# Optimization experiments

Measured on AMD Instinct MI355X. Metric: run time of the kernel, lower is better.

## Reference

```python
import jax, jax.numpy as jnp
import numpy as np

N = 100000      # nodes
E = 1600000     # edges
G = 64          # graphs in batch
H = 128         # hidden (== num_features)
L = 4           # num_layers
C = 16          # num_classes
NCAND = 100000  # candidate edges
BN_EPS = 1e-5


def setup_inputs() -> dict:
    key = jax.random.key(0)
    ks = jax.random.split(key, 24)
    s = 0.05
    inp = {}
    inp["x"] = jax.random.normal(ks[0], (N, H), dtype=jnp.float32)
    inp["edge_index"] = jax.random.randint(ks[1], (2, E), 0, N)
    inp["batch"] = jnp.sort(jax.random.randint(ks[2], (N,), 0, G))
    inp["candidate_edges"] = jax.random.randint(ks[3], (2, NCAND), 0, N)
    # GIN conv params, stacked over L layers (all layers are H->H since num_features==hidden)
    inp["cW1"] = jax.random.normal(ks[4], (L, H, H), dtype=jnp.float32) * s
    inp["cb1"] = jnp.zeros((L, H), jnp.float32)
    inp["cW2"] = jax.random.normal(ks[5], (L, H, H), dtype=jnp.float32) * s
    inp["cb2"] = jnp.zeros((L, H), jnp.float32)
    inp["cgamma"] = jnp.ones((L, H), jnp.float32)
    inp["cbeta"] = jnp.zeros((L, H), jnp.float32)
    inp["ceps"] = jnp.zeros((L,), jnp.float32)  # train_eps=True, init 0
    # node classifier: L*H -> 2H -> H -> H -> C (dropout is identity in eval)
    inp["ncW1"] = jax.random.normal(ks[6], (L * H, 2 * H), dtype=jnp.float32) * s
    inp["ncb1"] = jnp.zeros((2 * H,), jnp.float32)
    inp["ncW2"] = jax.random.normal(ks[7], (2 * H, H), dtype=jnp.float32) * s
    inp["ncb2"] = jnp.zeros((H,), jnp.float32)
    inp["ncW3"] = jax.random.normal(ks[8], (H, H), dtype=jnp.float32) * s
    inp["ncb3"] = jnp.zeros((H,), jnp.float32)
    inp["ncW4"] = jax.random.normal(ks[9], (H, C), dtype=jnp.float32) * s
    inp["ncb4"] = jnp.zeros((C,), jnp.float32)
    # edge predictor: 2*L*H -> 2H -> H -> 1
    inp["epW1"] = jax.random.normal(ks[10], (2 * L * H, 2 * H), dtype=jnp.float32) * s
    inp["epb1"] = jnp.zeros((2 * H,), jnp.float32)
    inp["epW2"] = jax.random.normal(ks[11], (2 * H, H), dtype=jnp.float32) * s
    inp["epb2"] = jnp.zeros((H,), jnp.float32)
    inp["epW3"] = jax.random.normal(ks[12], (H, 1), dtype=jnp.float32) * s
    inp["epb3"] = jnp.zeros((1,), jnp.float32)
    return inp


def _forward(x, cW1, cb1, cW2, cb2, cgamma, cbeta, ceps,
             ncW1, ncb1, ncW2, ncb2, ncW3, ncb3, ncW4, ncb4,
             epW1, epb1, epW2, epb2, epW3, epb3,
             edge_index, batch, candidate_edges):
    src, dst = edge_index[0], edge_index[1]
    h = x
    xs = []
    for l in range(L):
        # GIN: (1+eps)*x_i + sum_{j->i} x_j  (scatter-add over destination nodes)
        agg = jax.ops.segment_sum(h[src], dst, num_segments=N)
        z = (1.0 + ceps[l]) * h + agg
        z = jax.nn.relu(z @ cW1[l] + cb1[l])
        z = jax.nn.relu(z @ cW2[l] + cb2[l])
        # BatchNorm1d (training-mode batch statistics, biased variance)
        mu = z.mean(axis=0)
        var = jnp.var(z, axis=0)
        h = (z - mu) * jax.lax.rsqrt(var + BN_EPS) * cgamma[l] + cbeta[l]
        xs.append(h)
    emb = jnp.concatenate(xs, axis=-1)  # [N, L*H]
    # global mean pool over graphs
    sums = jax.ops.segment_sum(emb, batch, num_segments=G)
    cnt = jax.ops.segment_sum(jnp.ones((N, 1), emb.dtype), batch, num_segments=G)
    gemb = sums / jnp.maximum(cnt, 1.0)  # [G, L*H]
    t = jax.nn.relu(gemb @ ncW1 + ncb1)
    t = jax.nn.relu(t @ ncW2 + ncb2)
    t = jax.nn.relu(t @ ncW3 + ncb3)
    class_output = jax.nn.log_softmax(t @ ncW4 + ncb4, axis=1)  # [G, C]
    # link prediction: gather node embeddings per candidate edge
    ef = jnp.concatenate([emb[candidate_edges[0]], emb[candidate_edges[1]]], axis=1)  # [NC, 2*L*H]
    u = jax.nn.relu(ef @ epW1 + epb1)
    u = jax.nn.relu(u @ epW2 + epb2)
    edge_scores = jax.nn.sigmoid((u @ epW3 + epb3).squeeze(-1))  # [NC]
    return class_output, edge_scores


def reference(x, cW1, cb1, cW2, cb2, cgamma, cbeta, ceps,
              ncW1, ncb1, ncW2, ncb2, ncW3, ncb3, ncW4, ncb4,
              epW1, epb1, epW2, epb2, epW3, epb3,
              edge_index, batch, candidate_edges):
    return _forward(x, cW1, cb1, cW2, cb2, cgamma, cbeta, ceps,
                    ncW1, ncb1, ncW2, ncb2, ncW3, ncb3, ncW4, ncb4,
                    epW1, epb1, epW2, epb2, epW3, epb3,
                    edge_index, batch, candidate_edges)
```

## Files before the change

### kernel.cpp

```cpp
#include <hip/hip_runtime.h>
#include <math.h>

#define NN 100000
#define EE 1600000
#define GG 64
#define HH 128
#define LL 4
#define CCLS 16
#define NC 100000
#define NB 49
#define LDK 40
#define LDA2 136

typedef __attribute__((ext_vector_type(8))) short bf16x8;
typedef __attribute__((ext_vector_type(4))) float f32x4;

__device__ __forceinline__ unsigned short f2bf(float x) {
  union { float f; unsigned int u; } v; v.f = x;
  unsigned int r = v.u + 0x7fffu + ((v.u >> 16) & 1u);
  return (unsigned short)(r >> 16);
}
__device__ __forceinline__ float bl(unsigned u) {
  union { unsigned u; float f; } v; v.u = u << 16; return v.f;
}
__device__ __forceinline__ float bh(unsigned u) {
  union { unsigned u; float f; } v; v.u = u & 0xffff0000u; return v.f;
}

__global__ void hist_kernel(const int* __restrict__ dst, int* __restrict__ cnt, int E) {
  int e = blockIdx.x * 256 + threadIdx.x;
  if (e < E) atomicAdd(&cnt[dst[e]], 1);
}

__global__ __launch_bounds__(256) void scan_p1(const int* __restrict__ cnt,
                                               int* __restrict__ bsum, int n) {
  __shared__ int red[256];
  int tid = threadIdx.x;
  int base = blockIdx.x * 1024 + tid * 4;
  int s = 0;
  if (base + 3 < n) {
    int4 v = *(const int4*)(cnt + base);
    s = v.x + v.y + v.z + v.w;
  } else {
    for (int i = 0; i < 4; ++i) if (base + i < n) s += cnt[base + i];
  }
  red[tid] = s;
  __syncthreads();
  for (int st = 128; st >= 1; st >>= 1) {
    if (tid < st) red[tid] += red[tid + st];
    __syncthreads();
  }
  if (tid == 0) bsum[blockIdx.x] = red[0];
}

__global__ void scan_p2(int* __restrict__ bsum, int* __restrict__ rowptr,
                        int* __restrict__ bcursor, int nb, int n) {
  __shared__ int buf[128];
  int tid = threadIdx.x;
  int v = (tid < nb) ? bsum[tid] : 0;
  buf[tid] = v;
  __syncthreads();
  for (int off = 1; off < 128; off <<= 1) {
    int t = (tid >= off) ? buf[tid - off] : 0;
    __syncthreads();
    buf[tid] += t;
    __syncthreads();
  }
  if (tid < nb) bsum[tid] = buf[tid] - v;
  if (tid == 127) rowptr[n] = buf[127];
  __syncthreads();
  if (tid < NB) bcursor[tid] = bsum[2 * tid];
}

__global__ __launch_bounds__(256) void scan_p3(const int* __restrict__ cnt,
                                               const int* __restrict__ bsum,
                                               int* __restrict__ rowptr,
                                               int* __restrict__ cursor, int n) {
  __shared__ int red[256];
  int tid = threadIdx.x;
  int base = blockIdx.x * 1024 + tid * 4;
  int v[4] = {0, 0, 0, 0};
  if (base + 3 < n) {
    int4 t = *(const int4*)(cnt + base);
    v[0] = t.x; v[1] = t.y; v[2] = t.z; v[3] = t.w;
  } else {
    for (int i = 0; i < 4; ++i) if (base + i < n) v[i] = cnt[base + i];
  }
  int s = v[0] + v[1] + v[2] + v[3];
  red[tid] = s;
  __syncthreads();
  for (int off = 1; off < 256; off <<= 1) {
    int t = (tid >= off) ? red[tid - off] : 0;
    __syncthreads();
    red[tid] += t;
    __syncthreads();
  }
  int run = bsum[blockIdx.x] + red[tid] - s;
  int4 o;
  o.x = run; o.y = run + v[0]; o.z = o.y + v[1]; o.w = o.z + v[2];
  if (base + 3 < n) {
    *(int4*)(rowptr + base) = o;
    *(int4*)(cursor + base) = o;
  } else {
    int oo[4] = {o.x, o.y, o.z, o.w};
    for (int i = 0; i < 4; ++i)
      if (base + i < n) { rowptr[base + i] = oo[i]; cursor[base + i] = oo[i]; }
  }
}

__global__ __launch_bounds__(256) void partition_kernel(const int* __restrict__ src,
                                                        const int* __restrict__ dst,
                                                        int* __restrict__ bcursor,
                                                        int2* __restrict__ pairs, int E) {
  __shared__ int sS[4096];
  __shared__ int sD[4096];
  __shared__ int hist[NB];
  __shared__ int base[NB];
  int tid = threadIdx.x;
  int base_e = blockIdx.x * 4096;
  int cnt = min(4096, E - base_e);
  if (tid < NB) hist[tid] = 0;
  for (int i = tid * 4; i < cnt; i += 1024) {
    if (i + 3 < cnt) {
      *(int4*)(sS + i) = *(const int4*)(src + base_e + i);
      *(int4*)(sD + i) = *(const int4*)(dst + base_e + i);
    } else {
      for (int k = i; k < cnt; ++k) { sS[k] = src[base_e + k]; sD[k] = dst[base_e + k]; }
    }
  }
  __syncthreads();
  for (int i = tid; i < cnt; i += 256) atomicAdd(&hist[sD[i] >> 11], 1);
  __syncthreads();
  if (tid < NB) {
    base[tid] = atomicAdd(&bcursor[tid], hist[tid]);
    hist[tid] = 0;
  }
  __syncthreads();
  for (int i = tid; i < cnt; i += 256) {
    int d = sD[i];
    int b = d >> 11;
    int off = atomicAdd(&hist[b], 1);
    pairs[base[b] + off] = make_int2(sS[i], d);
  }
}

__global__ __launch_bounds__(256) void scatter_csr(const int2* __restrict__ pairs,
                                                   const int* __restrict__ rowptr,
                                                   int* __restrict__ cursor,
                                                   int* __restrict__ csr_src) {
  int b = blockIdx.x % 56;
  int slice = blockIdx.x / 56;
  if (b >= NB) return;
  int start = rowptr[b * 2048];
  int endn = min((b + 1) * 2048, NN);
  int end = rowptr[endn];
  for (int i = start + slice * 256 + threadIdx.x; i < end; i += 8 * 256) {
    int2 p = pairs[i];
    int pos = atomicAdd(&cursor[p.y], 1);
    csr_src[pos] = p.x;
  }
}

__global__ void f2b4_kernel(const float* __restrict__ in, unsigned short* __restrict__ out, int n4) {
  int i = blockIdx.x * 256 + threadIdx.x;
  if (i >= n4) return;
  float4 v = ((const float4*)in)[i];
  unsigned short r[4] = {f2bf(v.x), f2bf(v.y), f2bf(v.z), f2bf(v.w)};
  *(uint2*)(out + (size_t)i * 4) = *(uint2*)r;
}

__global__ void conv_weights(const float* __restrict__ cW1, const float* __restrict__ cW2,
                             unsigned short* __restrict__ WT1, unsigned short* __restrict__ WT2,
                             const float* __restrict__ epW1, unsigned short* __restrict__ W1T,
                             const float* __restrict__ epW2, unsigned short* __restrict__ W2T) {
  int idx = blockIdx.x * 256 + threadIdx.x;
  if (idx < LL * 16384) {
    int l = idx >> 14, r = idx & 16383, k = r >> 7, n = r & 127;
    WT1[l * 16384 + n * 128 + k] = f2bf(cW1[idx]);
    WT2[l * 16384 + n * 128 + k] = f2bf(cW2[idx]);
  } else if (idx < LL * 16384 + 262144) {
    int j = idx - LL * 16384;
    int k = j >> 8, n = j & 255;
    W1T[(size_t)n * 1024 + k] = f2bf(epW1[j]);
  } else if (idx < LL * 16384 + 262144 + 32768) {
    int j = idx - LL * 16384 - 262144;
    int k = j >> 7, n = j & 127;
    W2T[(size_t)n * 256 + k] = f2bf(epW2[j]);
  }
}

__global__ void aggregate_bf16(const unsigned short* __restrict__ h16, int ld,
                               const int* __restrict__ rowptr,
                               const int* __restrict__ csr_src,
                               const float* __restrict__ ceps_l,
                               unsigned short* __restrict__ out, int n) {
  int wave = threadIdx.x >> 6;
  int lane = threadIdx.x & 63;
  int sub = lane >> 4;
  int li = lane & 15;
  int node = blockIdx.x * 16 + wave * 4 + sub;
  if (node >= n) return;
  int c8 = li * 8;
  float eps1 = 1.0f + *ceps_l;
  float acc[8] = {};
  int b = rowptr[node], e = rowptr[node + 1];
  int j = b;
  for (; j + 8 <= e; j += 8) {
    uint4 u[8];
#pragma unroll
    for (int t = 0; t < 8; ++t) {
      int s = csr_src[j + t];
      u[t] = *(const uint4*)(h16 + (size_t)s * ld + c8);
    }
#pragma unroll
    for (int t = 0; t < 8; ++t) {
      acc[0] += bl(u[t].x); acc[1] += bh(u[t].x);
      acc[2] += bl(u[t].y); acc[3] += bh(u[t].y);
      acc[4] += bl(u[t].z); acc[5] += bh(u[t].z);
      acc[6] += bl(u[t].w); acc[7] += bh(u[t].w);
    }
  }
  for (; j < e; ++j) {
    int s = csr_src[j];
    uint4 u = *(const uint4*)(h16 + (size_t)s * ld + c8);
    acc[0] += bl(u.x); acc[1] += bh(u.x);
    acc[2] += bl(u.y); acc[3] += bh(u.y);
    acc[4] += bl(u.z); acc[5] += bh(u.z);
    acc[6] += bl(u.w); acc[7] += bh(u.w);
  }
  uint4 hu = *(const uint4*)(h16 + (size_t)node * ld + c8);
  acc[0] = fmaf(eps1, bl(hu.x), acc[0]); acc[1] = fmaf(eps1, bh(hu.x), acc[1]);
  acc[2] = fmaf(eps1, bl(hu.y), acc[2]); acc[3] = fmaf(eps1, bh(hu.y), acc[3]);
  acc[4] = fmaf(eps1, bl(hu.z), acc[4]); acc[5] = fmaf(eps1, bh(hu.z), acc[5]);
  acc[6] = fmaf(eps1, bl(hu.w), acc[6]); acc[7] = fmaf(eps1, bh(hu.w), acc[7]);
  unsigned short o[8];
#pragma unroll
  for (int i = 0; i < 8; ++i) o[i] = f2bf(acc[i]);
  *(uint4*)(out + (size_t)node * 128 + c8) = *(uint4*)o;
}

__global__ __launch_bounds__(256) void trunk_fused(
    const unsigned short* __restrict__ A16,
    const unsigned short* __restrict__ W1T, const float* __restrict__ b1,
    const unsigned short* __restrict__ W2T, const float* __restrict__ b2,
    float* __restrict__ bnsum, float* __restrict__ bnsumsq,
    unsigned short* __restrict__ C16, int M) {
  __shared__ unsigned short As[128 * LDA2];
  __shared__ unsigned short Bs[128 * LDK];
  const int tid = threadIdx.x;
  const int bm = blockIdx.x * 128;
  const int lane = tid & 63;
  const int wave = tid >> 6;
  const int wr = (wave >> 1) << 6;
  const int wc = (wave & 1) << 6;
  const int ar = tid >> 1;
  const int ah = (tid & 1) << 4;
  int gra = bm + ar; if (gra >= M) gra = M - 1;
  const unsigned short* Arow = A16 + (size_t)gra * 128;
  const int mrow = lane & 15;
  const int kq = (lane >> 4) << 3;
  f32x4 acc[4][4] = {};

#pragma unroll
  for (int ks = 0; ks < 4; ++ks) {
    const int k0 = ks << 5;
    const uint4* s = (const uint4*)(Arow + k0 + ah);
    *(uint4*)(As + ar * LDA2 + k0 + ah) = s[0];
    *(uint4*)(As + ar * LDA2 + k0 + ah + 8) = s[1];
  }
  uint4 p0 = *(const uint4*)(W1T + (size_t)ar * 128 + ah);
  uint4 p1 = *(const uint4*)(W1T + (size_t)ar * 128 + ah + 8);
  for (int ks = 0; ks < 4; ++ks) {
    const int k0 = ks << 5;
    *(uint4*)(Bs + ar * LDK + ah) = p0;
    *(uint4*)(Bs + ar * LDK + ah + 8) = p1;
    __syncthreads();
    if (ks < 3) {
      p0 = *(const uint4*)(W1T + (size_t)ar * 128 + k0 + 32 + ah);
      p1 = *(const uint4*)(W1T + (size_t)ar * 128 + k0 + 32 + ah + 8);
    }
    bf16x8 af[4], bfv[4];
#pragma unroll
    for (int t = 0; t < 4; ++t)
      af[t] = *(const bf16x8*)(As + (wr + t * 16 + mrow) * LDA2 + k0 + kq);
#pragma unroll
    for (int t = 0; t < 4; ++t)
      bfv[t] = *(const bf16x8*)(Bs + (wc + t * 16 + mrow) * LDK + kq);
#pragma unroll
    for (int mt = 0; mt < 4; ++mt)
#pragma unroll
      for (int nt = 0; nt < 4; ++nt)
        acc[mt][nt] = __builtin_amdgcn_mfma_f32_16x16x32_bf16(af[mt], bfv[nt], acc[mt][nt], 0, 0, 0);
    __syncthreads();
  }
  const int crow = (lane >> 4) << 2;
  const int ccol = lane & 15;
#pragma unroll
  for (int nt = 0; nt < 4; ++nt) {
    int c = wc + nt * 16 + ccol;
    float bz = b1[c];
#pragma unroll
    for (int mt = 0; mt < 4; ++mt) {
      int rl = wr + mt * 16 + crow;
#pragma unroll
      for (int i = 0; i < 4; ++i)
        As[(rl + i) * LDA2 + c] = f2bf(fmaxf(acc[mt][nt][i] + bz, 0.f));
    }
  }
#pragma unroll
  for (int mt = 0; mt < 4; ++mt)
#pragma unroll
    for (int nt = 0; nt < 4; ++nt)
      acc[mt][nt] = (f32x4){0.f, 0.f, 0.f, 0.f};
  p0 = *(const uint4*)(W2T + (size_t)ar * 128 + ah);
  p1 = *(const uint4*)(W2T + (size_t)ar * 128 + ah + 8);
  __syncthreads();
  for (int ks = 0; ks < 4; ++ks) {
    const int k0 = ks << 5;
    *(uint4*)(Bs + ar * LDK + ah) = p0;
    *(uint4*)(Bs + ar * LDK + ah + 8) = p1;
    __syncthreads();
    if (ks < 3) {
      p0 = *(const uint4*)(W2T + (size_t)ar * 128 + k0 + 32 + ah);
      p1 = *(const uint4*)(W2T + (size_t)ar * 128 + k0 + 32 + ah + 8);
    }
    bf16x8 af[4], bfv[4];
#pragma unroll
    for (int t = 0; t < 4; ++t)
      af[t] = *(const bf16x8*)(As + (wr + t * 16 + mrow) * LDA2 + k0 + kq);
#pragma unroll
    for (int t = 0; t < 4; ++t)
      bfv[t] = *(const bf16x8*)(Bs + (wc + t * 16 + mrow) * LDK + kq);
#pragma unroll
    for (int mt = 0; mt < 4; ++mt)
#pragma unroll
      for (int nt = 0; nt < 4; ++nt)
        acc[mt][nt] = __builtin_amdgcn_mfma_f32_16x16x32_bf16(af[mt], bfv[nt], acc[mt][nt], 0, 0, 0);
    __syncthreads();
  }
#pragma unroll
  for (int nt = 0; nt < 4; ++nt) {
    int c = wc + nt * 16 + ccol;
    float bz = b2[c];
    float s = 0.f, q = 0.f;
#pragma unroll
    for (int mt = 0; mt < 4; ++mt) {
      int rbase = bm + wr + mt * 16 + crow;
#pragma unroll
      for (int i = 0; i < 4; ++i) {
        int r = rbase + i;
        if (r < M) {
          float v = fmaxf(acc[mt][nt][i] + bz, 0.f);
          C16[(size_t)r * 128 + c] = f2bf(v);
          s += v; q += v * v;
        }
      }
    }
    s += __shfl_xor(s, 16, 64);
    s += __shfl_xor(s, 32, 64);
    q += __shfl_xor(q, 16, 64);
    q += __shfl_xor(q, 32, 64);
    if (lane < 16) {
      atomicAdd(&bnsum[c], s);
      atomicAdd(&bnsumsq[c], q);
    }
  }
}

__global__ __launch_bounds__(512) void mfma_gemm_gather(
    const unsigned short* __restrict__ emb16, const int* __restrict__ cand,
    const unsigned short* __restrict__ WT ,
    const float* __restrict__ bias,
    unsigned short* __restrict__ C16 , int M) {
  __shared__ unsigned short As[2][128 * LDK];
  __shared__ unsigned short Bs[2][256 * LDK];
  const int tid = threadIdx.x;
  const int bm = blockIdx.x * 128;
  const int lane = tid & 63;
  const int wave = tid >> 6;
  const int wr = (wave >> 2) << 6;
  const int wc = (wave & 3) << 6;
  f32x4 acc[4][4] = {};
  const int ar = tid >> 2;
  const int ah = (tid & 3) << 3;
  int gra = bm + ar; if (gra >= M) gra = M - 1;
  const int node0 = cand[gra];
  const int node1 = cand[NC + gra];
  const int br = tid >> 1;
  const int bh8 = (tid & 1) << 4;
  const unsigned short* Brow = WT + (size_t)br * 1024 + bh8;
  const int mrow = lane & 15;
  const int kq = (lane >> 4) << 3;

  {
    uint4 a = *(const uint4*)(emb16 + (size_t)node0 * 512 + ah);
    uint4 b0 = *(const uint4*)(Brow);
    uint4 b1 = *(const uint4*)(Brow + 8);
    *(uint4*)(As[0] + ar * LDK + ah) = a;
    *(uint4*)(Bs[0] + br * LDK + bh8) = b0;
    *(uint4*)(Bs[0] + br * LDK + bh8 + 8) = b1;
  }
  __syncthreads();
  for (int ks = 0; ks < 32; ++ks) {
    const int cur = ks & 1, nxt = cur ^ 1;
    uint4 a, b0, b1;
    if (ks < 31) {
      const int k1 = (ks + 1) << 5;
      int node = (k1 < 512) ? node0 : node1;
      a = *(const uint4*)(emb16 + (size_t)node * 512 + (k1 & 511) + ah);
      b0 = *(const uint4*)(Brow + k1);
      b1 = *(const uint4*)(Brow + k1 + 8);
    }
    bf16x8 af[4], bfv[4];
#pragma unroll
    for (int t = 0; t < 4; ++t)
      af[t] = *(const bf16x8*)(As[cur] + (wr + t * 16 + mrow) * LDK + kq);
#pragma unroll
    for (int t = 0; t < 4; ++t)
      bfv[t] = *(const bf16x8*)(Bs[cur] + (wc + t * 16 + mrow) * LDK + kq);
#pragma unroll
    for (int mt = 0; mt < 4; ++mt)
#pragma unroll
      for (int nt = 0; nt < 4; ++nt)
        acc[mt][nt] = __builtin_amdgcn_mfma_f32_16x16x32_bf16(af[mt], bfv[nt], acc[mt][nt], 0, 0, 0);
    if (ks < 31) {
      *(uint4*)(As[nxt] + ar * LDK + ah) = a;
      *(uint4*)(Bs[nxt] + br * LDK + bh8) = b0;
      *(uint4*)(Bs[nxt] + br * LDK + bh8 + 8) = b1;
      __syncthreads();
    }
  }
  const int crow = (lane >> 4) << 2;
  const int ccol = lane & 15;
#pragma unroll
  for (int nt = 0; nt < 4; ++nt) {
    int cbase = wc + nt * 16 + ccol;
    float bz = bias[cbase];
#pragma unroll
    for (int mt = 0; mt < 4; ++mt) {
      int rbase = bm + wr + mt * 16 + crow;
#pragma unroll
      for (int i = 0; i < 4; ++i) {
        int r = rbase + i;
        if (r < M) C16[(size_t)r * 256 + cbase] = f2bf(fmaxf(acc[mt][nt][i] + bz, 0.f));
      }
    }
  }
}

__global__ __launch_bounds__(256) void ep_gemm2_final(
    const unsigned short* __restrict__ A16 ,
    const unsigned short* __restrict__ WT ,
    const float* __restrict__ b2, const float* __restrict__ epW3,
    const float* __restrict__ epb3,
    float* __restrict__ out, int M) {
  __shared__ unsigned short As[2][128 * LDK];
  __shared__ unsigned short Bs[2][128 * LDK];
  __shared__ float sDot[128];
  const int tid = threadIdx.x;
  const int bm = blockIdx.x * 128;
  const int lane = tid & 63;
  const int wave = tid >> 6;
  const int wr = (wave >> 1) << 6;
  const int wc = (wave & 1) << 6;
  f32x4 acc[4][4] = {};
  const int ar = tid >> 1;
  const int ah = (tid & 1) << 4;
  int gra = bm + ar; if (gra >= M) gra = M - 1;
  const unsigned short* Arow = A16 + (size_t)gra * 256;
  const unsigned short* Brow = WT + (size_t)ar * 256;
  const int mrow = lane & 15;
  const int kq = (lane >> 4) << 3;

  if (tid < 128) sDot[tid] = 0.f;
  {
    uint4 a0 = *(const uint4*)(Arow + ah);
    uint4 a1 = *(const uint4*)(Arow + ah + 8);
    uint4 b0 = *(const uint4*)(Brow + ah);
    uint4 b1 = *(const uint4*)(Brow + ah + 8);
    *(uint4*)(As[0] + ar * LDK + ah) = a0;
    *(uint4*)(As[0] + ar * LDK + ah + 8) = a1;
    *(uint4*)(Bs[0] + ar * LDK + ah) = b0;
    *(uint4*)(Bs[0] + ar * LDK + ah + 8) = b1;
  }
  __syncthreads();
  for (int ks = 0; ks < 8; ++ks) {
    const int cur = ks & 1, nxt = cur ^ 1;
    uint4 a0, a1, b0, b1;
    if (ks < 7) {
      const int k1 = (ks + 1) << 5;
      a0 = *(const uint4*)(Arow + k1 + ah);
      a1 = *(const uint4*)(Arow + k1 + ah + 8);
      b0 = *(const uint4*)(Brow + k1 + ah);
      b1 = *(const uint4*)(Brow + k1 + ah + 8);
    }
    bf16x8 af[4], bfv[4];
#pragma unroll
    for (int t = 0; t < 4; ++t)
      af[t] = *(const bf16x8*)(As[cur] + (wr + t * 16 + mrow) * LDK + kq);
#pragma unroll
    for (int t = 0; t < 4; ++t)
      bfv[t] = *(const bf16x8*)(Bs[cur] + (wc + t * 16 + mrow) * LDK + kq);
#pragma unroll
    for (int mt = 0; mt < 4; ++mt)
#pragma unroll
      for (int nt = 0; nt < 4; ++nt)
        acc[mt][nt] = __builtin_amdgcn_mfma_f32_16x16x32_bf16(af[mt], bfv[nt], acc[mt][nt], 0, 0, 0);
    if (ks < 7) {
      *(uint4*)(As[nxt] + ar * LDK + ah) = a0;
      *(uint4*)(As[nxt] + ar * LDK + ah + 8) = a1;
      *(uint4*)(Bs[nxt] + ar * LDK + ah) = b0;
      *(uint4*)(Bs[nxt] + ar * LDK + ah + 8) = b1;
      __syncthreads();
    }
  }
  const int crow = (lane >> 4) << 2;
  const int ccol = lane & 15;
  float w3v[4], bz[4];
#pragma unroll
  for (int nt = 0; nt < 4; ++nt) {
    int c = wc + nt * 16 + ccol;
    w3v[nt] = epW3[c];
    bz[nt] = b2[c];
  }
  __syncthreads();
#pragma unroll
  for (int mt = 0; mt < 4; ++mt) {
#pragma unroll
    for (int i = 0; i < 4; ++i) {
      int rl = wr + mt * 16 + crow + i;
      float p = 0.f;
#pragma unroll
      for (int nt = 0; nt < 4; ++nt)
        p = fmaf(fmaxf(acc[mt][nt][i] + bz[nt], 0.f), w3v[nt], p);
      atomicAdd(&sDot[rl], p);
    }
  }
  __syncthreads();
  if (tid < 128) {
    int r = bm + tid;
    if (r < M) out[r] = 1.f / (1.f + expf(-(sDot[tid] + epb3[0])));
  }
}

__global__ void bn_apply_bf16(const unsigned short* __restrict__ z,
                              const float* __restrict__ sum, const float* __restrict__ sumsq,
                              const float* __restrict__ gamma, const float* __restrict__ beta,
                              unsigned short* __restrict__ out, int n) {
  int idx = blockIdx.x * 256 + threadIdx.x;
  if (idx >= n * 16) return;
  int r = idx >> 4, c8 = (idx & 15) << 3;
  uint4 v = *(const uint4*)(z + (size_t)r * 128 + c8);
  float f[8] = {bl(v.x), bh(v.x), bl(v.y), bh(v.y), bl(v.z), bh(v.z), bl(v.w), bh(v.w)};
  const float inv_n = 1.0f / (float)NN;
  unsigned short o[8];
#pragma unroll
  for (int j = 0; j < 8; ++j) {
    int c = c8 + j;
    float mu = sum[c] * inv_n;
    float var = sumsq[c] * inv_n - mu * mu;
    float sc = rsqrtf(var + 1e-5f) * gamma[c];
    o[j] = f2bf((f[j] - mu) * sc + beta[c]);
  }
  *(uint4*)(out + (size_t)r * 512 + c8) = *(uint4*)o;
}

__global__ void bounds_kernel(const int* __restrict__ batch, int* __restrict__ gstart, int n) {
  int g = threadIdx.x;
  if (g > GG) return;
  int lo = 0, hi = n;
  while (lo < hi) {
    int mid = (lo + hi) >> 1;
    if (batch[mid] < g) lo = mid + 1; else hi = mid;
  }
  gstart[g] = lo;
}

__global__ __launch_bounds__(256) void pool_bf16(const unsigned short* __restrict__ emb16,
                                                 const int* __restrict__ gstart,
                                                 float* __restrict__ gsum) {
  int g = blockIdx.x;
  int chunk = blockIdx.y;
  int c2 = threadIdx.x * 2;
  int s = gstart[g], e = gstart[g + 1];
  int len = e - s;
  int per = (len + 7) >> 3;
  int r0 = s + chunk * per;
  int r1 = min(r0 + per, e);
  float ax = 0.f, ay = 0.f;
  for (int r = r0; r < r1; ++r) {
    unsigned u = *(const unsigned*)(emb16 + (size_t)r * 512 + c2);
    ax += bl(u); ay += bh(u);
  }
  if (r1 > r0) {
    atomicAdd(&gsum[g * 512 + c2], ax);
    atomicAdd(&gsum[g * 512 + c2 + 1], ay);
  }
}

__global__ __launch_bounds__(256) void nc_fused(
    const float* __restrict__ gsum, const int* __restrict__ gstart,
    const float* __restrict__ W1, const float* __restrict__ b1,
    const float* __restrict__ W2, const float* __restrict__ b2,
    const float* __restrict__ W3, const float* __restrict__ b3,
    const float* __restrict__ W4, const float* __restrict__ b4,
    float* __restrict__ out) {
  __shared__ float row[512];
  __shared__ float t1[256];
  __shared__ float t2[128];
  __shared__ float t3s[128];
  __shared__ float lg[16];
  int g = blockIdx.x;
  int tid = threadIdx.x;
  float inv = 1.0f / fmaxf((float)(gstart[g + 1] - gstart[g]), 1.0f);
  row[tid] = gsum[g * 512 + tid] * inv;
  row[tid + 256] = gsum[g * 512 + tid + 256] * inv;
  __syncthreads();
  {
    float acc = b1[tid];
#pragma unroll 8
    for (int k = 0; k < 512; ++k) acc = fmaf(row[k], W1[k * 256 + tid], acc);
    t1[tid] = fmaxf(acc, 0.f);
  }
  __syncthreads();
  if (tid < 128) {
    float acc = b2[tid];
#pragma unroll 8
    for (int k = 0; k < 256; ++k) acc = fmaf(t1[k], W2[k * 128 + tid], acc);
    t2[tid] = fmaxf(acc, 0.f);
  }
  __syncthreads();
  if (tid < 128) {
    float acc = b3[tid];
#pragma unroll 8
    for (int k = 0; k < 128; ++k) acc = fmaf(t2[k], W3[k * 128 + tid], acc);
    t3s[tid] = fmaxf(acc, 0.f);
  }
  __syncthreads();
  if (tid < 16) {
    float acc = b4[tid];
#pragma unroll 8
    for (int k = 0; k < 128; ++k) acc = fmaf(t3s[k], W4[k * 16 + tid], acc);
    lg[tid] = acc;
  }
  __syncthreads();
  if (tid < 16) {
    float v = lg[tid];
    float m = v;
    for (int j = 0; j < 16; ++j) m = fmaxf(m, lg[j]);
    float s = 0.f;
    for (int j = 0; j < 16; ++j) s += expf(lg[j] - m);
    out[g * 16 + tid] = v - m - logf(s);
  }
}

extern "C" void kernel_launch(void* const* d_in, const int* in_sizes, int n_in,
                              void* d_out, int out_size, void* d_ws, size_t ws_size,
                              hipStream_t stream) {
  const float* x = (const float*)d_in[0];
  const int* edge_index = (const int*)d_in[1];
  const int* batch = (const int*)d_in[2];
  const int* cand = (const int*)d_in[3];
  const float* cW1 = (const float*)d_in[4];
  const float* cb1 = (const float*)d_in[5];
  const float* cW2 = (const float*)d_in[6];
  const float* cb2 = (const float*)d_in[7];
  const float* cgamma = (const float*)d_in[8];
  const float* cbeta = (const float*)d_in[9];
  const float* ceps = (const float*)d_in[10];
  const float* ncW1 = (const float*)d_in[11];
  const float* ncb1 = (const float*)d_in[12];
  const float* ncW2 = (const float*)d_in[13];
  const float* ncb2 = (const float*)d_in[14];
  const float* ncW3 = (const float*)d_in[15];
  const float* ncb3 = (const float*)d_in[16];
  const float* ncW4 = (const float*)d_in[17];
  const float* ncb4 = (const float*)d_in[18];
  const float* epW1 = (const float*)d_in[19];
  const float* epb1 = (const float*)d_in[20];
  const float* epW2 = (const float*)d_in[21];
  const float* epb2 = (const float*)d_in[22];
  const float* epW3 = (const float*)d_in[23];
  const float* epb3 = (const float*)d_in[24];

  char* ws = (char*)d_ws;
  size_t off = 0;
  auto alloc = [&](size_t bytes) -> void* {
    off = (off + 255) & ~(size_t)255;
    void* p = ws + off;
    off += bytes;
    return p;
  };
  size_t zz_bytes = (size_t)NN * 4 + 512 * 4 + 512 * 4 + (size_t)GG * 512 * 4;
  char* zz = (char*)alloc(zz_bytes);
  int* cnt = (int*)zz;
  float* bnsum = (float*)(zz + (size_t)NN * 4);
  float* bnsumsq = bnsum + 512;
  float* gsum = bnsumsq + 512;
  int* rowptr = (int*)alloc((size_t)(NN + 1) * 4);
  int* cursor = (int*)alloc((size_t)NN * 4);
  int* csr_src = (int*)alloc((size_t)EE * 4);
  int2* pairs = (int2*)alloc((size_t)EE * 8);
  int* bsum = (int*)alloc(128 * 4);
  int* bcursor = (int*)alloc(64 * 4);
  unsigned short* x16 = (unsigned short*)alloc((size_t)NN * 128 * 2);
  unsigned short* g16a = (unsigned short*)alloc((size_t)NN * 128 * 2);
  unsigned short* emb16 = (unsigned short*)alloc((size_t)NN * 512 * 2);
  unsigned short* C1 = (unsigned short*)alloc((size_t)NC * 256 * 2);
  unsigned short* WT1 = (unsigned short*)alloc((size_t)LL * 16384 * 2);
  unsigned short* WT2 = (unsigned short*)alloc((size_t)LL * 16384 * 2);
  unsigned short* W1T = (unsigned short*)alloc((size_t)1024 * 256 * 2);
  unsigned short* W2T = (unsigned short*)alloc((size_t)256 * 128 * 2);
  int* gstart = (int*)alloc(65 * 4);

  const int* esrc = edge_index;
  const int* edst = edge_index + EE;
  const int nblk = (NN + 1023) / 1024;
  const int nech = (EE + 4095) / 4096;

  hipMemsetAsync(zz, 0, zz_bytes, stream);
  hist_kernel<<<(EE + 255) / 256, 256, 0, stream>>>(edst, cnt, EE);
  scan_p1<<<nblk, 256, 0, stream>>>(cnt, bsum, NN);
  scan_p2<<<1, 128, 0, stream>>>(bsum, rowptr, bcursor, nblk, NN);
  scan_p3<<<nblk, 256, 0, stream>>>(cnt, bsum, rowptr, cursor, NN);
  partition_kernel<<<nech, 256, 0, stream>>>(esrc, edst, bcursor, pairs, EE);
  scatter_csr<<<56 * 8, 256, 0, stream>>>(pairs, rowptr, cursor, csr_src);
  f2b4_kernel<<<(NN * 128 / 4 + 255) / 256, 256, 0, stream>>>(x, x16, NN * 128 / 4);
  conv_weights<<<(LL * 16384 + 262144 + 32768 + 255) / 256, 256, 0, stream>>>(
      cW1, cW2, WT1, WT2, epW1, W1T, epW2, W2T);

  for (int l = 0; l < LL; ++l) {
    const unsigned short* h16 = (l == 0) ? x16 : (emb16 + (size_t)(l - 1) * 128);
    int ld = (l == 0) ? 128 : 512;
    aggregate_bf16<<<(NN + 15) / 16, 256, 0, stream>>>(h16, ld, rowptr, csr_src, ceps + l, g16a, NN);
    trunk_fused<<<(NN + 127) / 128, 256, 0, stream>>>(
        g16a, WT1 + (size_t)l * 16384, cb1 + l * 128,
        WT2 + (size_t)l * 16384, cb2 + l * 128,
        bnsum + l * 128, bnsumsq + l * 128, g16a, NN);
    bn_apply_bf16<<<(NN * 16 + 255) / 256, 256, 0, stream>>>(
        g16a, bnsum + l * 128, bnsumsq + l * 128, cgamma + l * 128, cbeta + l * 128,
        emb16 + (size_t)l * 128, NN);
  }

  bounds_kernel<<<1, 128, 0, stream>>>(batch, gstart, NN);
  pool_bf16<<<dim3(GG, 8), 256, 0, stream>>>(emb16, gstart, gsum);
  nc_fused<<<GG, 256, 0, stream>>>(gsum, gstart, ncW1, ncb1, ncW2, ncb2, ncW3, ncb3,
                                   ncW4, ncb4, (float*)d_out);

  mfma_gemm_gather<<<(NC + 127) / 128, 512, 0, stream>>>(emb16, cand, W1T, epb1, C1, NC);
  ep_gemm2_final<<<(NC + 127) / 128, 256, 0, stream>>>(C1, W2T, epb2, epW3, epb3,
                                                       (float*)d_out + GG * CCLS, NC);
}
```

Before: 1.120 ms.

## Fuse edge-predictor GEMM1 and GEMM2 into one kernel via shared-memory intermediate

Merges the gathered first edge-predictor GEMM with the second GEMM and final dot/sigmoid into a single kernel. The 128x256 bf16 hidden tile is kept in shared memory, reusing the GEMM1 staging buffers, instead of being written to and re-read from a global intermediate buffer. That removes a kernel launch and roughly 100 MB of global traffic. In exchange, GEMM2 now reads its B operand straight from global memory (likely L2 resident) without double buffering, and the larger shared-memory footprint may reduce occupancy.

```diff
diff --git a/kernel.cpp b/kernel.cpp
--- a/kernel.cpp
+++ b/kernel.cpp
@@ -11,6 +11,7 @@
 #define NB 49
 #define LDK 40
 #define LDA2 136
+#define LDC 260
 
 typedef __attribute__((ext_vector_type(8))) short bf16x8;
 typedef __attribute__((ext_vector_type(4))) float f32x4;
@@ -367,13 +368,18 @@
   }
 }
 
-__global__ __launch_bounds__(512) void mfma_gemm_gather(
+__global__ __launch_bounds__(512) void ep_fused(
     const unsigned short* __restrict__ emb16, const int* __restrict__ cand,
-    const unsigned short* __restrict__ WT ,
-    const float* __restrict__ bias,
-    unsigned short* __restrict__ C16 , int M) {
-  __shared__ unsigned short As[2][128 * LDK];
-  __shared__ unsigned short Bs[2][256 * LDK];
+    const unsigned short* __restrict__ W1T ,
+    const float* __restrict__ b1,
+    const unsigned short* __restrict__ W2T ,
+    const float* __restrict__ b2, const float* __restrict__ epW3,
+    const float* __restrict__ epb3,
+    float* __restrict__ out, int M) {
+  __shared__ unsigned short smem[128 * LDC];
+  __shared__ float sDot[128];
+  const int AOFF = 0;
+  const int BOFF = 2 * 128 * LDK;
   const int tid = threadIdx.x;
   const int bm = blockIdx.x * 128;
   const int lane = tid & 63;
@@ -388,151 +394,103 @@
   const int node1 = cand[NC + gra];
   const int br = tid >> 1;
   const int bh8 = (tid & 1) << 4;
-  const unsigned short* Brow = WT + (size_t)br * 1024 + bh8;
+  const unsigned short* Brow = W1T + (size_t)br * 1024 + bh8;
   const int mrow = lane & 15;
   const int kq = (lane >> 4) << 3;
 
+  if (tid < 128) sDot[tid] = 0.f;
   {
     uint4 a = *(const uint4*)(emb16 + (size_t)node0 * 512 + ah);
     uint4 b0 = *(const uint4*)(Brow);
-    uint4 b1 = *(const uint4*)(Brow + 8);
-    *(uint4*)(As[0] + ar * LDK + ah) = a;
-    *(uint4*)(Bs[0] + br * LDK + bh8) = b0;
-    *(uint4*)(Bs[0] + br * LDK + bh8 + 8) = b1;
+    uint4 b1v = *(const uint4*)(Brow + 8);
+    *(uint4*)(smem + AOFF + ar * LDK + ah) = a;
+    *(uint4*)(smem + BOFF + br * LDK + bh8) = b0;
+    *(uint4*)(smem + BOFF + br * LDK + bh8 + 8) = b1v;
   }
   __syncthreads();
   for (int ks = 0; ks < 32; ++ks) {
-    const int cur = ks & 1, nxt = cur ^ 1;
-    uint4 a, b0, b1;
+    const int cur = ks & 1;
+    unsigned short* Ac = smem + AOFF + cur * (128 * LDK);
+    unsigned short* Bc = smem + BOFF + cur * (256 * LDK);
+    unsigned short* An = smem + AOFF + (cur ^ 1) * (128 * LDK);
+    unsigned short* Bn = smem + BOFF + (cur ^ 1) * (256 * LDK);
+    uint4 a, b0, b1v;
     if (ks < 31) {
       const int k1 = (ks + 1) << 5;
       int node = (k1 < 512) ? node0 : node1;
       a = *(const uint4*)(emb16 + (size_t)node * 512 + (k1 & 511) + ah);
       b0 = *(const uint4*)(Brow + k1);
-      b1 = *(const uint4*)(Brow + k1 + 8);
+      b1v = *(const uint4*)(Brow + k1 + 8);
     }
     bf16x8 af[4], bfv[4];
 #pragma unroll
     for (int t = 0; t < 4; ++t)
-      af[t] = *(const bf16x8*)(As[cur] + (wr + t * 16 + mrow) * LDK + kq);
+      af[t] = *(const bf16x8*)(Ac + (wr + t * 16 + mrow) * LDK + kq);
 #pragma unroll
     for (int t = 0; t < 4; ++t)
-      bfv[t] = *(const bf16x8*)(Bs[cur] + (wc + t * 16 + mrow) * LDK + kq);
+      bfv[t] = *(const bf16x8*)(Bc + (wc + t * 16 + mrow) * LDK + kq);
 #pragma unroll
     for (int mt = 0; mt < 4; ++mt)
 #pragma unroll
       for (int nt = 0; nt < 4; ++nt)
         acc[mt][nt] = __builtin_amdgcn_mfma_f32_16x16x32_bf16(af[mt], bfv[nt], acc[mt][nt], 0, 0, 0);
     if (ks < 31) {
-      *(uint4*)(As[nxt] + ar * LDK + ah) = a;
-      *(uint4*)(Bs[nxt] + br * LDK + bh8) = b0;
-      *(uint4*)(Bs[nxt] + br * LDK + bh8 + 8) = b1;
+      *(uint4*)(An + ar * LDK + ah) = a;
+      *(uint4*)(Bn + br * LDK + bh8) = b0;
+      *(uint4*)(Bn + br * LDK + bh8 + 8) = b1v;
       __syncthreads();
     }
   }
+  __syncthreads();
   const int crow = (lane >> 4) << 2;
   const int ccol = lane & 15;
 #pragma unroll
   for (int nt = 0; nt < 4; ++nt) {
-    int cbase = wc + nt * 16 + ccol;
-    float bz = bias[cbase];
+    int c = wc + nt * 16 + ccol;
+    float bz = b1[c];
 #pragma unroll
     for (int mt = 0; mt < 4; ++mt) {
-      int rbase = bm + wr + mt * 16 + crow;
-#pragma unroll
-      for (int i = 0; i < 4; ++i) {
-        int r = rbase + i;
-        if (r < M) C16[(size_t)r * 256 + cbase] = f2bf(fmaxf(acc[mt][nt][i] + bz, 0.f));
-      }
-    }
-  }
-}
-
-__global__ __launch_bounds__(256) void ep_gemm2_final(
-    const unsigned short* __restrict__ A16 ,
-    const unsigned short* __restrict__ WT ,
-    const float* __restrict__ b2, const float* __restrict__ epW3,
-    const float* __restrict__ epb3,
-    float* __restrict__ out, int M) {
-  __shared__ unsigned short As[2][128 * LDK];
-  __shared__ unsigned short Bs[2][128 * LDK];
-  __shared__ float sDot[128];
-  const int tid = threadIdx.x;
-  const int bm = blockIdx.x * 128;
-  const int lane = tid & 63;
-  const int wave = tid >> 6;
-  const int wr = (wave >> 1) << 6;
-  const int wc = (wave & 1) << 6;
-  f32x4 acc[4][4] = {};
-  const int ar = tid >> 1;
-  const int ah = (tid & 1) << 4;
-  int gra = bm + ar; if (gra >= M) gra = M - 1;
-  const unsigned short* Arow = A16 + (size_t)gra * 256;
-  const unsigned short* Brow = WT + (size_t)ar * 256;
-  const int mrow = lane & 15;
-  const int kq = (lane >> 4) << 3;
-
-  if (tid < 128) sDot[tid] = 0.f;
-  {
-    uint4 a0 = *(const uint4*)(Arow + ah);
-    uint4 a1 = *(const uint4*)(Arow + ah + 8);
-    uint4 b0 = *(const uint4*)(Brow + ah);
-    uint4 b1 = *(const uint4*)(Brow + ah + 8);
-    *(uint4*)(As[0] + ar * LDK + ah) = a0;
-    *(uint4*)(As[0] + ar * LDK + ah + 8) = a1;
-    *(uint4*)(Bs[0] + ar * LDK + ah) = b0;
-    *(uint4*)(Bs[0] + ar * LDK + ah + 8) = b1;
-  }
-  __syncthreads();
+      int rl = wr + mt * 16 + crow;
+#pragma unroll
+      for (int i = 0; i < 4; ++i)
+        smem[(rl + i) * LDC + c] = f2bf(fmaxf(acc[mt][nt][i] + bz, 0.f));
+    }
+  }
+  __syncthreads();
+  const int wr2 = (wave >> 1) << 5;
+  const int wc2 = (wave & 1) << 6;
+  f32x4 acc2[2][4] = {};
   for (int ks = 0; ks < 8; ++ks) {
-    const int cur = ks & 1, nxt = cur ^ 1;
-    uint4 a0, a1, b0, b1;
-    if (ks < 7) {
-      const int k1 = (ks + 1) << 5;
-      a0 = *(const uint4*)(Arow + k1 + ah);
-      a1 = *(const uint4*)(Arow + k1 + ah + 8);
-      b0 = *(const uint4*)(Brow + k1 + ah);
-      b1 = *(const uint4*)(Brow + k1 + ah + 8);
-    }
-    bf16x8 af[4], bfv[4];
+    const int k0 = ks << 5;
+    bf16x8 af[2], bfv[4];
+#pragma unroll
+    for (int t = 0; t < 2; ++t)
+      af[t] = *(const bf16x8*)(smem + (wr2 + t * 16 + mrow) * LDC + k0 + kq);
 #pragma unroll
     for (int t = 0; t < 4; ++t)
-      af[t] = *(const bf16x8*)(As[cur] + (wr + t * 16 + mrow) * LDK + kq);
-#pragma unroll
-    for (int t = 0; t < 4; ++t)
-      bfv[t] = *(const bf16x8*)(Bs[cur] + (wc + t * 16 + mrow) * LDK + kq);
-#pragma unroll
-    for (int mt = 0; mt < 4; ++mt)
+      bfv[t] = *(const bf16x8*)(W2T + (size_t)(wc2 + t * 16 + mrow) * 256 + k0 + kq);
+#pragma unroll
+    for (int mt = 0; mt < 2; ++mt)
 #pragma unroll
       for (int nt = 0; nt < 4; ++nt)
-        acc[mt][nt] = __builtin_amdgcn_mfma_f32_16x16x32_bf16(af[mt], bfv[nt], acc[mt][nt], 0, 0, 0);
-    if (ks < 7) {
-      *(uint4*)(As[nxt] + ar * LDK + ah) = a0;
-      *(uint4*)(As[nxt] + ar * LDK + ah + 8) = a1;
-      *(uint4*)(Bs[nxt] + ar * LDK + ah) = b0;
-      *(uint4*)(Bs[nxt] + ar * LDK + ah + 8) = b1;
-      __syncthreads();
-    }
-  }
-  const int crow = (lane >> 4) << 2;
-  const int ccol = lane & 15;
-  float w3v[4], bz[4];
+        acc2[mt][nt] = __builtin_amdgcn_mfma_f32_16x16x32_bf16(af[mt], bfv[nt], acc2[mt][nt], 0, 0, 0);
+  }
+  float w3v[4], bz2[4];
 #pragma unroll
   for (int nt = 0; nt < 4; ++nt) {
-    int c = wc + nt * 16 + ccol;
+    int c = wc2 + nt * 16 + ccol;
     w3v[nt] = epW3[c];
-    bz[nt] = b2[c];
-  }
-  __syncthreads();
-#pragma unroll
-  for (int mt = 0; mt < 4; ++mt) {
+    bz2[nt] = b2[c];
+  }
+#pragma unroll
+  for (int mt = 0; mt < 2; ++mt) {
 #pragma unroll
     for (int i = 0; i < 4; ++i) {
-      int rl = wr + mt * 16 + crow + i;
+      int rl = wr2 + mt * 16 + crow + i;
       float p = 0.f;
 #pragma unroll
       for (int nt = 0; nt < 4; ++nt)
-        p = fmaf(fmaxf(acc[mt][nt][i] + bz[nt], 0.f), w3v[nt], p);
+        p = fmaf(fmaxf(acc2[mt][nt][i] + bz2[nt], 0.f), w3v[nt], p);
       atomicAdd(&sDot[rl], p);
     }
   }
@@ -706,7 +664,6 @@
   unsigned short* x16 = (unsigned short*)alloc((size_t)NN * 128 * 2);
   unsigned short* g16a = (unsigned short*)alloc((size_t)NN * 128 * 2);
   unsigned short* emb16 = (unsigned short*)alloc((size_t)NN * 512 * 2);
-  unsigned short* C1 = (unsigned short*)alloc((size_t)NC * 256 * 2);
   unsigned short* WT1 = (unsigned short*)alloc((size_t)LL * 16384 * 2);
   unsigned short* WT2 = (unsigned short*)alloc((size_t)LL * 16384 * 2);
   unsigned short* W1T = (unsigned short*)alloc((size_t)1024 * 256 * 2);
@@ -747,7 +704,7 @@
   nc_fused<<<GG, 256, 0, stream>>>(gsum, gstart, ncW1, ncb1, ncW2, ncb2, ncW3, ncb3,
                                    ncW4, ncb4, (float*)d_out);
 
-  mfma_gemm_gather<<<(NC + 127) / 128, 512, 0, stream>>>(emb16, cand, W1T, epb1, C1, NC);
-  ep_gemm2_final<<<(NC + 127) / 128, 256, 0, stream>>>(C1, W2T, epb2, epW3, epb3,
-                                                       (float*)d_out + GG * CCLS, NC);
-}
+  ep_fused<<<(NC + 127) / 128, 512, 0, stream>>>(
+      emb16, cand, W1T, epb1, W2T, epb2, epW3, epb3,
+      (float*)d_out + GG * CCLS, NC);
+}
```

Result: no change. 1.106 ms (-1.3%).
